# Performance work log

Hardware: AMD Instinct MI355X
Metric: run time of the kernel (lower is better)

## Reference

```python
import jax, jax.numpy as jnp
import numpy as np

N_NODES = 50000
N_EDGES = 800000
IN_C, HID_C, OUT_C = 128, 128, 64
BN_EPS = 1e-5


def setup_inputs() -> dict:
    key = jax.random.key(0)
    ks = jax.random.split(key, 12)
    def lin(k, fan_in, fan_out):
        bound = 1.0 / np.sqrt(fan_in)
        kw, kb = jax.random.split(k)
        W = jax.random.uniform(kw, (fan_in, fan_out), jnp.float32, -bound, bound)
        b = jax.random.uniform(kb, (fan_out,), jnp.float32, -bound, bound)
        return W, b
    x = jax.random.normal(ks[0], (N_NODES, IN_C), jnp.float32)
    edge_index = jax.random.randint(ks[1], (2, N_EDGES), 0, N_NODES, jnp.int32)
    w1a, b1a = lin(ks[2], IN_C, HID_C)
    w1b, b1b = lin(ks[3], HID_C, HID_C)
    w2a, b2a = lin(ks[4], HID_C, OUT_C)
    w2b, b2b = lin(ks[5], OUT_C, OUT_C)
    return {
        "x": x, "edge_index": edge_index,
        "w1a": w1a, "b1a": b1a, "g1": jnp.ones((HID_C,)), "be1": jnp.zeros((HID_C,)),
        "w1b": w1b, "b1b": b1b,
        "w2a": w2a, "b2a": b2a, "g2": jnp.ones((OUT_C,)), "be2": jnp.zeros((OUT_C,)),
        "w2b": w2b, "b2b": b2b,
    }


def _batchnorm(h, gamma, beta):
    # training-style BN over node dim, biased variance (torch BatchNorm1d)
    mean = jnp.mean(h, axis=0)
    var = jnp.mean(jnp.square(h - mean), axis=0)
    return (h - mean) * jax.lax.rsqrt(var + BN_EPS) * gamma + beta


def _gin_layer(x, src, dst, n_nodes, w_a, b_a, gamma, beta, w_b, b_b):
    # GINConv with eps=0: MLP(x + sum_{j->i} x_j)
    agg = jax.ops.segment_sum(x[src], dst, num_segments=n_nodes)  # [N, C]
    h = x + agg
    h = h @ w_a + b_a
    h = jax.nn.relu(_batchnorm(h, gamma, beta))
    return h @ w_b + b_b


def reference(x, edge_index, w1a, b1a, g1, be1, w1b, b1b, w2a, b2a, g2, be2, w2b, b2b):
    src, dst = edge_index[0], edge_index[1]
    n = x.shape[0]
    h = _gin_layer(x, src, dst, n, w1a, b1a, g1, be1, w1b, b1b)
    h = jax.nn.relu(h)  # dropout p=0.0 -> identity
    h = _gin_layer(h, src, dst, n, w2a, b2a, g2, be2, w2b, b2b)
    return jax.nn.log_softmax(h, axis=-1)
```

## Files before the change

### kernel.cpp

```cpp
#include <hip/hip_runtime.h>


typedef unsigned short u16;
typedef unsigned int u32;
typedef __attribute__((ext_vector_type(8))) short short8;
typedef __attribute__((ext_vector_type(4))) short short4v;
typedef __attribute__((ext_vector_type(4))) float f32x4;

#define DEV_INLINE __device__ __forceinline__

DEV_INLINE void atomAddF(float* p, float v) { unsafeAtomicAdd(p, v); }

DEV_INLINE u16 f2bf(float f) {
    unsigned u = __float_as_uint(f);
    u += 0x7fffu + ((u >> 16) & 1u);
    return (u16)(u >> 16);
}
DEV_INLINE float bf2f(u16 h) { return __uint_as_float(((unsigned)h) << 16); }

__global__ __launch_bounds__(256) void wprep4_k(
    const float* __restrict__ w1a, const float* __restrict__ w1b,
    const float* __restrict__ w2a, const float* __restrict__ w2b,
    short* __restrict__ o1a, short* __restrict__ o1b,
    short* __restrict__ o2a, short* __restrict__ o2b)
{
    int b = blockIdx.x;
    const float* W; short* wf; int K, NOUT;
    if (b < 8)       { W = w1a; wf = o1a; K = 128; NOUT = 128; }
    else if (b < 16) { W = w1b; wf = o1b; K = 128; NOUT = 128; b -= 8; }
    else if (b < 20) { W = w2a; wf = o2a; K = 128; NOUT = 64;  b -= 16; }
    else             { W = w2b; wf = o2b; K = 64;  NOUT = 64;  b -= 20; }
    const int u = b * 256 + threadIdx.x;
    const int units = (NOUT / 16) * (K / 32) * 64;
    if (u >= units) return;
    const int per_ct = (K / 32) * 64;
    const int ct = u / per_ct;
    const int rem = u % per_ct;
    const int kc = rem >> 6;
    const int l = rem & 63;
    const int col = ct * 16 + (l & 15);
    const int k0 = kc * 32 + (l >> 4) * 8;
    short8 pk;
#pragma unroll
    for (int j = 0; j < 8; j++)
        pk[j] = (short)f2bf(W[(size_t)(k0 + j) * NOUT + col]);
    *(short8*)&wf[(size_t)u * 8] = pk;
}

template <int KD, int NC, bool ABF16, bool BNIN, bool BIAS, bool RELUOUT,
          bool LOGSM, bool OBF16>
__global__ __launch_bounds__(256) void mgemm(
    const void* __restrict__ Ap, const short* __restrict__ Wf,
    const float* __restrict__ sum, const float* __restrict__ sumsq,
    const float* __restrict__ g, const float* __restrict__ be, float invN,
    const float* __restrict__ bias, void* __restrict__ outp, int M)
{
    constexpr int BM = 64;
    constexpr int KC = KD / 32;
    constexpr int CT = NC / 16;
    constexpr int KQ = KD / 4;
    __shared__ short Asl[BM * KD];
    __shared__ short Bsl[NC * KD];
    __shared__ float scb[BNIN ? KD : 1];
    __shared__ float shb[BNIN ? KD : 1];

    const int t = threadIdx.x;
    const int l = t & 63;
    const int w = t >> 6;

    if constexpr (BNIN) {
        if (t < KD) {
            const float m = sum[t] * invN;
            const float v = sumsq[t] * invN - m * m;
            const float r = rsqrtf(v + 1e-5f);
            const float s = g[t] * r;
            scb[t] = s;
            shb[t] = be[t] - m * s;
        }
        __syncthreads();
    }

    {
        const float4* src = (const float4*)Wf;
        float4* dst = (float4*)Bsl;
        constexpr int NU = NC * KD / 8;
#pragma unroll
        for (int u = t; u < NU; u += 256) dst[u] = src[u];
    }
    {
        const int r = t >> 2;
        const int q = t & 3;
        const int grow = blockIdx.x * BM + r;
        const int rt = r >> 4;
        u16 hv[KQ];
        if (grow < M) {
            if constexpr (ABF16) {
                const u16* ap = (const u16*)Ap + (size_t)grow * KD + q * KQ;
#pragma unroll
                for (int i = 0; i < KQ / 8; i++)
                    *(short8*)&hv[i * 8] = ((const short8*)ap)[i];
                if constexpr (BNIN) {
#pragma unroll
                    for (int i = 0; i < KQ; i++) {
                        const int k = q * KQ + i;
                        hv[i] = f2bf(fmaxf(0.f, bf2f(hv[i]) * scb[k] + shb[k]));
                    }
                }
            } else {
                const float* ap = (const float*)Ap + (size_t)grow * KD + q * KQ;
#pragma unroll
                for (int i = 0; i < KQ / 4; i++) {
                    const float4 v = ((const float4*)ap)[i];
                    float f0 = v.x, f1 = v.y, f2 = v.z, f3 = v.w;
                    if constexpr (BNIN) {
                        const int k = q * KQ + i * 4;
                        f0 = fmaxf(0.f, f0 * scb[k + 0] + shb[k + 0]);
                        f1 = fmaxf(0.f, f1 * scb[k + 1] + shb[k + 1]);
                        f2 = fmaxf(0.f, f2 * scb[k + 2] + shb[k + 2]);
                        f3 = fmaxf(0.f, f3 * scb[k + 3] + shb[k + 3]);
                    }
                    hv[i * 4 + 0] = f2bf(f0); hv[i * 4 + 1] = f2bf(f1);
                    hv[i * 4 + 2] = f2bf(f2); hv[i * 4 + 3] = f2bf(f3);
                }
            }
        } else {
#pragma unroll
            for (int i = 0; i < KQ; i++) hv[i] = 0;
        }
#pragma unroll
        for (int gg = 0; gg < KQ / 8; gg++) {
            const int k0 = q * KQ + gg * 8;
            const int kc = k0 >> 5;
            const int lane = (r & 15) + ((k0 >> 3) & 3) * 16;
            *(short8*)&Asl[((rt * KC + kc) * 64 + lane) * 8] =
                *(short8*)&hv[gg * 8];
        }
    }
    __syncthreads();

    f32x4 acc[CT];
#pragma unroll
    for (int c = 0; c < CT; c++) acc[c] = (f32x4){0.f, 0.f, 0.f, 0.f};

#pragma unroll
    for (int kc = 0; kc < KC; kc++) {
        const short8 x0 = *(const short8*)&Asl[((w * KC + kc) * 64 + l) * 8];
#pragma unroll
        for (int ct = 0; ct < CT; ct++) {
            const short8 wb = *(const short8*)&Bsl[((ct * KC + kc) * 64 + l) * 8];
            acc[ct] = __builtin_amdgcn_mfma_f32_16x16x32_bf16(wb, x0, acc[ct], 0, 0, 0);
        }
    }

    const int cbase = (l >> 4) * 4;
    const int grow = blockIdx.x * BM + w * 16 + (l & 15);
    if constexpr (!LOGSM) {
        if (grow < M) {
#pragma unroll
            for (int ct = 0; ct < CT; ct++) {
                f32x4 o = acc[ct];
                if constexpr (BIAS) {
                    const float4 bv = *(const float4*)&bias[ct * 16 + cbase];
                    o[0] += bv.x; o[1] += bv.y; o[2] += bv.z; o[3] += bv.w;
                }
                if constexpr (RELUOUT) {
#pragma unroll
                    for (int j = 0; j < 4; j++) o[j] = fmaxf(o[j], 0.f);
                }
                if constexpr (OBF16) {
                    short4v o16;
#pragma unroll
                    for (int j = 0; j < 4; j++) o16[j] = (short)f2bf(o[j]);
                    *(short4v*)&((u16*)outp)[(size_t)grow * NC + ct * 16 + cbase] = o16;
                } else {
                    *(f32x4*)&((float*)outp)[(size_t)grow * NC + ct * 16 + cbase] = o;
                }
            }
        }
    } else {
        float v[CT * 4];
#pragma unroll
        for (int ct = 0; ct < CT; ct++) {
            const float4 bv = *(const float4*)&bias[ct * 16 + cbase];
            v[ct * 4 + 0] = acc[ct][0] + bv.x;
            v[ct * 4 + 1] = acc[ct][1] + bv.y;
            v[ct * 4 + 2] = acc[ct][2] + bv.z;
            v[ct * 4 + 3] = acc[ct][3] + bv.w;
        }
        float m = v[0];
#pragma unroll
        for (int j = 1; j < CT * 4; j++) m = fmaxf(m, v[j]);
        m = fmaxf(m, __shfl_xor(m, 16));
        m = fmaxf(m, __shfl_xor(m, 32));
        float s = 0.f;
#pragma unroll
        for (int j = 0; j < CT * 4; j++) s += __expf(v[j] - m);
        s += __shfl_xor(s, 16);
        s += __shfl_xor(s, 32);
        const float lg = m + __logf(s);
        if (grow < M) {
#pragma unroll
            for (int ct = 0; ct < CT; ct++) {
                f32x4 o;
#pragma unroll
                for (int j = 0; j < 4; j++) o[j] = v[ct * 4 + j] - lg;
                *(f32x4*)&((float*)outp)[(size_t)grow * NC + ct * 16 + cbase] = o;
            }
        }
    }
}

__global__ __launch_bounds__(256) void hist_k(const int* __restrict__ ei,
                                              int* __restrict__ cnt, int E)
{
    const int gid = blockIdx.x * blockDim.x + threadIdx.x;
    const int stride = gridDim.x * blockDim.x;
    for (int e = gid; e < E; e += stride) atomicAdd(&cnt[ei[E + e]], 1);
}

__global__ __launch_bounds__(256) void bsum_k(const int* __restrict__ cnt,
                                              int* __restrict__ bsum, int N)
{
    __shared__ int ws[4];
    const int i = blockIdx.x * 256 + threadIdx.x;
    int v = (i < N) ? cnt[i] : 0;
    for (int d = 32; d; d >>= 1) v += __shfl_xor(v, d, 64);
    if ((threadIdx.x & 63) == 0) ws[threadIdx.x >> 6] = v;
    __syncthreads();
    if (threadIdx.x == 0) bsum[blockIdx.x] = ws[0] + ws[1] + ws[2] + ws[3];
}

__global__ __launch_bounds__(256) void bscan_k(const int* __restrict__ bsum,
                                               int* __restrict__ bpre, int G1)
{
    __shared__ int part[256];
    const int t = threadIdx.x;
    const int v = (t < G1) ? bsum[t] : 0;
    part[t] = v;
    __syncthreads();
    for (int d = 1; d < 256; d <<= 1) {
        const int u = (t >= d) ? part[t - d] : 0;
        __syncthreads();
        part[t] += u;
        __syncthreads();
    }
    bpre[t] = part[t] - v;
}

__global__ __launch_bounds__(256) void offs_k(const int* __restrict__ cnt,
                                              const int* __restrict__ bpre,
                                              int* __restrict__ off,
                                              int* __restrict__ cursor,
                                              int N, int E)
{
    __shared__ int part[256];
    const int t = threadIdx.x;
    const int i = blockIdx.x * 256 + t;
    const int v = (i < N) ? cnt[i] : 0;
    part[t] = v;
    __syncthreads();
    for (int d = 1; d < 256; d <<= 1) {
        const int u = (t >= d) ? part[t - d] : 0;
        __syncthreads();
        part[t] += u;
        __syncthreads();
    }
    if (i < N) {
        const int o = bpre[blockIdx.x] + part[t] - v;
        off[i] = o;
        cursor[i] = o;
    }
    if (blockIdx.x == 0 && t == 0) off[N] = E;
}

__global__ __launch_bounds__(256) void fill_k(const int* __restrict__ ei,
                                              int* __restrict__ cursor,
                                              int* __restrict__ srcs, int E)
{
    const int gid = blockIdx.x * blockDim.x + threadIdx.x;
    const int stride = gridDim.x * blockDim.x;
    for (int e = gid; e < E; e += stride) {
        const int s = ei[e];
        const int d = ei[E + e];
        const int pos = atomicAdd(&cursor[d], 1);
        srcs[pos] = s;
    }
}

template <int C>
__global__ __launch_bounds__(256) void segsum_bf(
    const u16* __restrict__ p, const int* __restrict__ off,
    const int* __restrict__ srcs, u16* __restrict__ out,
    float* __restrict__ sum, float* __restrict__ sumsq, int N)
{
    constexpr int BLKN = 8;
    constexpr int VPL = C / 64;
    __shared__ float red[4][64][2 * VPL];

    const int wv = threadIdx.x >> 6;
    const int l  = threadIdx.x & 63;
    const int base = blockIdx.x * 4 * BLKN;

    float ss[VPL], qq[VPL];
#pragma unroll
    for (int v = 0; v < VPL; v++) { ss[v] = 0.f; qq[v] = 0.f; }

    for (int i = 0; i < BLKN; i++) {
        const int n = base + i * 4 + wv;
        if (n < N) {
            const int lo = __builtin_amdgcn_readfirstlane(off[n]);
            const int hi = __builtin_amdgcn_readfirstlane(off[n + 1]);
            float acc[VPL];
            if constexpr (VPL == 2) {
                const u32 u = *(const u32*)&p[(size_t)n * C + 2 * l];
                acc[0] = bf2f((u16)u);
                acc[1] = bf2f((u16)(u >> 16));
            } else {
                acc[0] = bf2f(p[(size_t)n * C + l]);
            }
            const int cnt = hi - lo;
            if (cnt > 0) {
                const int last = hi - 1;
                int idx[8];
#pragma unroll
                for (int j = 0; j < 8; j++) idx[j] = srcs[min(lo + j, last)];
                for (int e = lo; e < hi; e += 8) {
                    int nx[8];
#pragma unroll
                    for (int j = 0; j < 8; j++)
                        nx[j] = srcs[min(e + 8 + j, last)];
#pragma unroll
                    for (int j = 0; j < 8; j++) {
                        const bool live = (e + j) < hi;
                        if constexpr (VPL == 2) {
                            const u32 u = *(const u32*)&p[(size_t)idx[j] * C + 2 * l];
                            const float v0 = bf2f((u16)u);
                            const float v1 = bf2f((u16)(u >> 16));
                            acc[0] += live ? v0 : 0.f;
                            acc[1] += live ? v1 : 0.f;
                        } else {
                            const float v = bf2f(p[(size_t)idx[j] * C + l]);
                            acc[0] += live ? v : 0.f;
                        }
                    }
#pragma unroll
                    for (int j = 0; j < 8; j++) idx[j] = nx[j];
                }
            }
            if constexpr (VPL == 2) {
                const u16 r0 = f2bf(acc[0]);
                const u16 r1 = f2bf(acc[1]);
                *(u32*)&out[(size_t)n * C + 2 * l] = (u32)r0 | ((u32)r1 << 16);
                const float f0 = bf2f(r0), f1 = bf2f(r1);
                ss[0] += f0; qq[0] += f0 * f0;
                ss[1] += f1; qq[1] += f1 * f1;
            } else {
                const u16 r = f2bf(acc[0]);
                out[(size_t)n * C + l] = r;
                const float f = bf2f(r);
                ss[0] += f; qq[0] += f * f;
            }
        }
    }

#pragma unroll
    for (int v = 0; v < VPL; v++) {
        red[wv][l][2 * v] = ss[v];
        red[wv][l][2 * v + 1] = qq[v];
    }
    __syncthreads();
    if (wv == 0) {
#pragma unroll
        for (int v = 0; v < VPL; v++) {
            float a = 0.f, b = 0.f;
#pragma unroll
            for (int w2 = 0; w2 < 4; w2++) {
                a += red[w2][l][2 * v];
                b += red[w2][l][2 * v + 1];
            }
            const int ch = (VPL == 2) ? (2 * l + v) : l;
            atomAddF(&sum[ch], a);
            atomAddF(&sumsq[ch], b);
        }
    }
}

extern "C" void kernel_launch(void* const* d_in, const int* in_sizes, int n_in,
                              void* d_out, int out_size, void* d_ws, size_t ws_size,
                              hipStream_t stream)
{
    const float* x   = (const float*)d_in[0];
    const int*   ei  = (const int*)d_in[1];
    const float* w1a = (const float*)d_in[2];
    const float* g1  = (const float*)d_in[4];
    const float* be1 = (const float*)d_in[5];
    const float* w1b = (const float*)d_in[6];
    const float* b1b = (const float*)d_in[7];
    const float* w2a = (const float*)d_in[8];
    const float* g2  = (const float*)d_in[10];
    const float* be2 = (const float*)d_in[11];
    const float* w2b = (const float*)d_in[12];
    const float* b2b = (const float*)d_in[13];
    float* out = (float*)d_out;

    const int N = in_sizes[0] / 128;
    const int E = in_sizes[1] / 2;

    u16* buf1 = (u16*)d_ws;
    u16* buf2 = buf1 + (size_t)N * 128;
    float* stats = (float*)(buf2 + (size_t)N * 128);
    float* sum1 = stats,       *sq1 = stats + 128;
    float* sum2 = stats + 256, *sq2 = stats + 320;
    int* cnt    = (int*)(stats + 1024);
    int* off    = cnt + N;
    int* cursor = off + N + 1;
    int* srcs   = cursor + N;
    int* bsum   = srcs + E;
    int* bpre   = bsum + 256;
    short* w1af = (short*)(bpre + 256);
    short* w1bf = w1af + 128 * 128;
    short* w2af = w1bf + 128 * 128;
    short* w2bf = w2af + 128 * 64;
    u16* p1 = buf1;
    u16* s1 = buf2;
    u16* h1 = buf1;
    u16* p2 = buf2;
    u16* s2 = buf2 + (size_t)N * 64;

    hipMemsetAsync(stats, 0, 1024 * sizeof(float) + (size_t)N * sizeof(int), stream);

    const int G1 = (N + 255) / 256;
    const int gb = (N + 63) / 64;
    const int gs = (N + 31) / 32;
    const float invN = 1.f / N;

    hist_k<<<1024, 256, 0, stream>>>(ei, cnt, E);
    bsum_k<<<G1, 256, 0, stream>>>(cnt, bsum, N);
    bscan_k<<<1, 256, 0, stream>>>(bsum, bpre, G1);
    offs_k<<<G1, 256, 0, stream>>>(cnt, bpre, off, cursor, N, E);
    fill_k<<<1024, 256, 0, stream>>>(ei, cursor, srcs, E);

    wprep4_k<<<22, 256, 0, stream>>>(w1a, w1b, w2a, w2b, w1af, w1bf, w2af, w2bf);

    mgemm<128, 128, false, false, false, false, false, true>
        <<<gb, 256, 0, stream>>>(x, w1af, nullptr, nullptr, nullptr, nullptr,
                                 0.f, nullptr, p1, N);
    segsum_bf<128><<<gs, 256, 0, stream>>>(p1, off, srcs, s1, sum1, sq1, N);
    mgemm<128, 128, true, true, true, true, false, true>
        <<<gb, 256, 0, stream>>>(s1, w1bf, sum1, sq1, g1, be1, invN, b1b, h1, N);

    mgemm<128, 64, true, false, false, false, false, true>
        <<<gb, 256, 0, stream>>>(h1, w2af, nullptr, nullptr, nullptr, nullptr,
                                 0.f, nullptr, p2, N);
    segsum_bf<64><<<gs, 256, 0, stream>>>(p2, off, srcs, s2, sum2, sq2, N);
    mgemm<64, 64, true, true, true, false, true, false>
        <<<gb, 256, 0, stream>>>(s2, w2bf, sum2, sq2, g2, be2, invN, b2b, out, N);
}
```

Before: 302.1 us.

## Fuse layer-1 output GEMM with layer-2 input GEMM via shared memory

Adds a kernel that applies BN+ReLU to the aggregated layer-1 features, multiplies by w1b, applies bias+ReLU, and keeps the intermediate tile in a swizzled LDS layout so it can be multiplied by w2a right away. The separate launch is gone, and the full N×128 bf16 h1 buffer is no longer written and read back. The segment-sum block size is also halved (BLKN 8→4, twice as many blocks), which raises parallelism at the cost of more stat-reduction atomics. In exchange, the fused kernel uses more LDS per block, which may lower occupancy.

After: 395.0 us. 30.8% more time.

```diff
diff --git a/kernel.cpp b/kernel.cpp
--- a/kernel.cpp
+++ b/kernel.cpp
@@ -210,6 +210,143 @@
     }
 }
 
+__global__ __launch_bounds__(256) void mgemm23_k(
+    const u16* __restrict__ s1, const short* __restrict__ w1bf,
+    const short* __restrict__ w2af,
+    const float* __restrict__ sum, const float* __restrict__ sumsq,
+    const float* __restrict__ g, const float* __restrict__ be, float invN,
+    const float* __restrict__ b1b, u16* __restrict__ p2, int M)
+{
+    constexpr int BM = 64, KD = 128, NC = 128, NO = 64;
+    constexpr int KC = KD / 32;
+    constexpr int CT = NC / 16;
+    constexpr int CT2 = NO / 16;
+    constexpr int KQ = KD / 4;
+    __shared__ short Asl[BM * KD];
+    __shared__ short Bsl[NC * KD];
+    __shared__ float scb[KD];
+    __shared__ float shb[KD];
+
+    const int t = threadIdx.x;
+    const int l = t & 63;
+    const int w = t >> 6;
+
+    if (t < KD) {
+        const float m = sum[t] * invN;
+        const float v = sumsq[t] * invN - m * m;
+        const float r = rsqrtf(v + 1e-5f);
+        const float s = g[t] * r;
+        scb[t] = s;
+        shb[t] = be[t] - m * s;
+    }
+    __syncthreads();
+
+    {
+        const float4* src = (const float4*)w1bf;
+        float4* dst = (float4*)Bsl;
+#pragma unroll
+        for (int u = t; u < NC * KD / 8; u += 256) dst[u] = src[u];
+    }
+    {
+        const int r = t >> 2;
+        const int q = t & 3;
+        const int grow = blockIdx.x * BM + r;
+        const int rt = r >> 4;
+        u16 hv[KQ];
+        if (grow < M) {
+            const u16* ap = s1 + (size_t)grow * KD + q * KQ;
+#pragma unroll
+            for (int i = 0; i < KQ / 8; i++)
+                *(short8*)&hv[i * 8] = ((const short8*)ap)[i];
+#pragma unroll
+            for (int i = 0; i < KQ; i++) {
+                const int k = q * KQ + i;
+                hv[i] = f2bf(fmaxf(0.f, bf2f(hv[i]) * scb[k] + shb[k]));
+            }
+        } else {
+#pragma unroll
+            for (int i = 0; i < KQ; i++) hv[i] = 0;
+        }
+#pragma unroll
+        for (int gg = 0; gg < KQ / 8; gg++) {
+            const int k0 = q * KQ + gg * 8;
+            const int kc = k0 >> 5;
+            const int lane = (r & 15) + ((k0 >> 3) & 3) * 16;
+            *(short8*)&Asl[((rt * KC + kc) * 64 + lane) * 8] =
+                *(short8*)&hv[gg * 8];
+        }
+    }
+    __syncthreads();
+
+    f32x4 acc[CT];
+#pragma unroll
+    for (int c = 0; c < CT; c++) acc[c] = (f32x4){0.f, 0.f, 0.f, 0.f};
+#pragma unroll
+    for (int kc = 0; kc < KC; kc++) {
+        const short8 x0 = *(const short8*)&Asl[((w * KC + kc) * 64 + l) * 8];
+#pragma unroll
+        for (int ct = 0; ct < CT; ct++) {
+            const short8 wb = *(const short8*)&Bsl[((ct * KC + kc) * 64 + l) * 8];
+            acc[ct] = __builtin_amdgcn_mfma_f32_16x16x32_bf16(wb, x0, acc[ct], 0, 0, 0);
+        }
+    }
+    __syncthreads();
+
+    {
+        const int row = w * 16 + (l & 15);
+        const int cb4 = l >> 4;
+        const int sw = (row & 7) << 1;
+#pragma unroll
+        for (int ct = 0; ct < CT; ct++) {
+            const float4 bv = *(const float4*)&b1b[ct * 16 + cb4 * 4];
+            short4v o16;
+            o16[0] = (short)f2bf(fmaxf(acc[ct][0] + bv.x, 0.f));
+            o16[1] = (short)f2bf(fmaxf(acc[ct][1] + bv.y, 0.f));
+            o16[2] = (short)f2bf(fmaxf(acc[ct][2] + bv.z, 0.f));
+            o16[3] = (short)f2bf(fmaxf(acc[ct][3] + bv.w, 0.f));
+            const int gsw = (ct * 4 + cb4) ^ sw;
+            *(short4v*)&Asl[row * 128 + gsw * 4] = o16;
+        }
+    }
+    {
+        const float4* src = (const float4*)w2af;
+        float4* dst = (float4*)Bsl;
+#pragma unroll
+        for (int u = t; u < NO * KD / 8; u += 256) dst[u] = src[u];
+    }
+    __syncthreads();
+
+    f32x4 acc2[CT2];
+#pragma unroll
+    for (int c = 0; c < CT2; c++) acc2[c] = (f32x4){0.f, 0.f, 0.f, 0.f};
+#pragma unroll
+    for (int kc = 0; kc < KC; kc++) {
+        const int row = w * 16 + (l & 15);
+        const int G = kc * 8 + (l >> 4) * 2;
+        const int Gs = G ^ ((row & 7) << 1);
+        const short8 x0 = *(const short8*)&Asl[row * 128 + Gs * 4];
+#pragma unroll
+        for (int ct = 0; ct < CT2; ct++) {
+            const short8 wb = *(const short8*)&Bsl[((ct * KC + kc) * 64 + l) * 8];
+            acc2[ct] = __builtin_amdgcn_mfma_f32_16x16x32_bf16(wb, x0, acc2[ct], 0, 0, 0);
+        }
+    }
+
+    {
+        const int cbase = (l >> 4) * 4;
+        const int grow = blockIdx.x * BM + w * 16 + (l & 15);
+        if (grow < M) {
+#pragma unroll
+            for (int ct = 0; ct < CT2; ct++) {
+                short4v o16;
+#pragma unroll
+                for (int j = 0; j < 4; j++) o16[j] = (short)f2bf(acc2[ct][j]);
+                *(short4v*)&p2[(size_t)grow * NO + ct * 16 + cbase] = o16;
+            }
+        }
+    }
+}
+
 __global__ __launch_bounds__(256) void hist_k(const int* __restrict__ ei,
                                               int* __restrict__ cnt, int E)
 {
@@ -293,7 +430,7 @@
     const int* __restrict__ srcs, u16* __restrict__ out,
     float* __restrict__ sum, float* __restrict__ sumsq, int N)
 {
-    constexpr int BLKN = 8;
+    constexpr int BLKN = 4;
     constexpr int VPL = C / 64;
     __shared__ float red[4][64][2 * VPL];
 
@@ -423,15 +560,14 @@
     short* w2bf = w2af + 128 * 64;
     u16* p1 = buf1;
     u16* s1 = buf2;
-    u16* h1 = buf1;
-    u16* p2 = buf2;
-    u16* s2 = buf2 + (size_t)N * 64;
+    u16* p2 = buf1;
+    u16* s2 = buf2;
 
     hipMemsetAsync(stats, 0, 1024 * sizeof(float) + (size_t)N * sizeof(int), stream);
 
     const int G1 = (N + 255) / 256;
     const int gb = (N + 63) / 64;
-    const int gs = (N + 31) / 32;
+    const int gs = (N + 15) / 16;
     const float invN = 1.f / N;
 
     hist_k<<<1024, 256, 0, stream>>>(ei, cnt, E);
@@ -446,12 +582,10 @@
         <<<gb, 256, 0, stream>>>(x, w1af, nullptr, nullptr, nullptr, nullptr,
                                  0.f, nullptr, p1, N);
     segsum_bf<128><<<gs, 256, 0, stream>>>(p1, off, srcs, s1, sum1, sq1, N);
-    mgemm<128, 128, true, true, true, true, false, true>
-        <<<gb, 256, 0, stream>>>(s1, w1bf, sum1, sq1, g1, be1, invN, b1b, h1, N);
-
-    mgemm<128, 64, true, false, false, false, false, true>
-        <<<gb, 256, 0, stream>>>(h1, w2af, nullptr, nullptr, nullptr, nullptr,
-                                 0.f, nullptr, p2, N);
+
+    mgemm23_k<<<gb, 256, 0, stream>>>(s1, w1bf, w2af, sum1, sq1, g1, be1,
+                                      invN, b1b, p2, N);
+
     segsum_bf<64><<<gs, 256, 0, stream>>>(p2, off, srcs, s2, sum2, sq2, N);
     mgemm<64, 64, true, true, true, false, true, false>
         <<<gb, 256, 0, stream>>>(s2, w2bf, sum2, sq2, g2, be2, invN, b2b, out, N);
```
